# Kernel tuning notes

Measured on AMD Instinct MI355X. Metric: run time of the kernel, lower is better.

Reference implementation:

```python
import jax, jax.numpy as jnp
import numpy as np


def _binarize(x):
    # tf.where(x < 0, -1.0, 1.0)
    return jnp.where(x < 0, -1.0, 1.0).astype(jnp.float32)


def setup_inputs() -> dict:
    key = jax.random.key(0)
    k1, k2, k3 = jax.random.split(key, 3)
    M, K, N = 8192, 2048, 2048
    inputs = jax.random.normal(k1, (M, K), dtype=jnp.float32)
    kernel = jax.random.normal(k2, (K, N), dtype=jnp.float32) * 0.1
    bias = jax.random.normal(k3, (N,), dtype=jnp.float32) * 0.01
    return {"inputs": inputs, "kernel": kernel, "bias": bias}


def reference(inputs, kernel, bias):
    bx = _binarize(inputs)          # [M, K] in {-1, +1}
    bw = _binarize(kernel)          # [K, N] in {-1, +1}
    return jnp.matmul(bx, bw) + bias  # [M, N]
```

## Files before the change

### kernel.cpp

```cpp
#include <hip/hip_runtime.h>
#include <stdint.h>

typedef __attribute__((ext_vector_type(4))) int int4v;
typedef __attribute__((ext_vector_type(8))) int int8v;
typedef __attribute__((ext_vector_type(4))) float floatx4;
typedef __attribute__((ext_vector_type(16))) unsigned char uchar16;

#define MDIM 8192
#define KDIM 2048
#define NDIM 2048
#define BM 256
#define BN 256
#define KB 1024
#define BKB 128
#define NT 8

__device__ __forceinline__ void load16_lds(const void* g, void* l) {
  __builtin_amdgcn_global_load_lds(
      (const __attribute__((address_space(1))) void*)g,
      (__attribute__((address_space(3))) void*)l, 16, 0, 0);
}

#define XBLK 2048
#define WBLK 512

__global__ void binarize_fused(const float* __restrict__ X,
                               const float* __restrict__ W,
                               unsigned char* __restrict__ Xb,
                               unsigned char* __restrict__ WbT) {
  const int b = blockIdx.x;
  if (b < XBLK) {
    size_t i = ((size_t)b * 256 + threadIdx.x) * 32;
    const float4* xp = (const float4*)(X + i);
    uchar16 o;
#pragma unroll
    for (int h = 0; h < 8; ++h) {
      float4 a = xp[h];
      unsigned n0 = (a.x < 0.f) ? 0xAu : 0x2u;
      unsigned n1 = (a.y < 0.f) ? 0xAu : 0x2u;
      unsigned n2 = (a.z < 0.f) ? 0xAu : 0x2u;
      unsigned n3 = (a.w < 0.f) ? 0xAu : 0x2u;
      o[2 * h]     = (unsigned char)(n0 | (n1 << 4));
      o[2 * h + 1] = (unsigned char)(n2 | (n3 << 4));
    }
    *(uchar16*)(Xb + i / 2) = o;
  } else {
    const int bw = b - XBLK;
    const int nb = bw & 31;
    const int kb = bw >> 5;
    const int nn = threadIdx.x & 63;
    const int kc = kb * 4 + (threadIdx.x >> 6);
    const float* wp = W + (size_t)(kc * 32) * NDIM + nb * 64 + nn;
    uchar16 o;
#pragma unroll
    for (int j = 0; j < 16; ++j) {
      unsigned lo = (wp[(size_t)(2 * j) * NDIM] < 0.f) ? 0xAu : 0x2u;
      unsigned hi = (wp[(size_t)(2 * j + 1) * NDIM] < 0.f) ? 0xAu : 0x2u;
      o[j] = (unsigned char)(lo | (hi << 4));
    }
    *(uchar16*)(WbT + (size_t)(nb * 64 + nn) * KB + kc * 16) = o;
  }
}

__global__ __launch_bounds__(512, 2) void gemm_bin_fp4(
    const unsigned char* __restrict__ A,
    const unsigned char* __restrict__ B,
    const float* __restrict__ bias,
    float* __restrict__ C) {
  __shared__ __align__(16) unsigned char As[2][BM * BKB];
  __shared__ __align__(16) unsigned char Bs[2][BN * BKB];

  const int tid = threadIdx.x;
  const int lane = tid & 63;
  const int wv = tid >> 6;
  const int wm = wv >> 2;
  const int wn = wv & 3;
  const int r = lane & 15;
  const int q = lane >> 4;

  const int m0 = blockIdx.x * BM;
  const int n0 = blockIdx.y * BN;

  floatx4 acc[8][4] = {};

  const int qbase = wv * 256;
  int srcoff[4];
#pragma unroll
  for (int i = 0; i < 4; ++i) {
    const int s = qbase + i * 64 + lane;
    const int row = s >> 3;
    const int cg = (s & 7) ^ (row & 7);
    srcoff[i] = row * KB + cg * 16;
  }
  const unsigned char* Ab = A + (size_t)m0 * KB;
  const unsigned char* Bb = B + (size_t)n0 * KB;

#pragma unroll
  for (int i = 0; i < 4; ++i) {
    load16_lds(Ab + srcoff[i], &As[0][(qbase + i * 64) * 16]);
    load16_lds(Bb + srcoff[i], &Bs[0][(qbase + i * 64) * 16]);
  }

  for (int t = 0; t < NT; ++t) {
    const int cur = t & 1;
    if (t < NT - 1) {
      const int kbb = (t + 1) * BKB;
#pragma unroll
      for (int i = 0; i < 4; ++i) {
        load16_lds(Ab + kbb + srcoff[i], &As[cur ^ 1][(qbase + i * 64) * 16]);
        load16_lds(Bb + kbb + srcoff[i], &Bs[cur ^ 1][(qbase + i * 64) * 16]);
      }
      asm volatile("s_waitcnt vmcnt(8)" ::: "memory");
    } else {
      asm volatile("s_waitcnt vmcnt(0)" ::: "memory");
    }
    __builtin_amdgcn_s_barrier();

#pragma unroll
    for (int s2 = 0; s2 < 2; ++s2) {
      int8v b8[4];
#pragma unroll
      for (int tn = 0; tn < 4; ++tn) {
        const int brow = wn * 64 + tn * 16 + r;
        int4v bv = *(const int4v*)(&Bs[cur][brow * BKB + (((s2 * 4 + q) ^ (r & 7)) * 16)]);
        b8[tn] = int8v{bv[0], bv[1], bv[2], bv[3], 0, 0, 0, 0};
      }
#pragma unroll
      for (int tm = 0; tm < 8; ++tm) {
        const int arow = wm * 128 + tm * 16 + r;
        int4v av = *(const int4v*)(&As[cur][arow * BKB + (((s2 * 4 + q) ^ (r & 7)) * 16)]);
        int8v a8 = int8v{av[0], av[1], av[2], av[3], 0, 0, 0, 0};
#pragma unroll
        for (int tn = 0; tn < 4; ++tn)
          acc[tm][tn] = __builtin_amdgcn_mfma_scale_f32_16x16x128_f8f6f4(
              a8, b8[tn], acc[tm][tn], 4, 4,
              0, 0x7F7F7F7F, 0, 0x7F7F7F7F);
      }
    }
    asm volatile("s_waitcnt lgkmcnt(0)" ::: "memory");
    __builtin_amdgcn_s_barrier();
  }

  __syncthreads();
  float* slab = (float*)(&As[0][0]) + wv * 1024;

  float bv[4];
#pragma unroll
  for (int tn = 0; tn < 4; ++tn) bv[tn] = bias[n0 + wn * 64 + tn * 16 + r];

  const int lrow = lane >> 4;
  const int lc4 = lane & 15;

#pragma unroll
  for (int tm = 0; tm < 8; ++tm) {
#pragma unroll
    for (int tn = 0; tn < 4; ++tn)
#pragma unroll
      for (int v = 0; v < 4; ++v)
        slab[(q * 4 + v) * 64 + tn * 16 + r] = acc[tm][tn][v] + bv[tn];
    asm volatile("s_waitcnt lgkmcnt(0)" ::: "memory");
    __builtin_amdgcn_sched_barrier(0);
#pragma unroll
    for (int j = 0; j < 4; ++j) {
      const int row = j * 4 + lrow;
      floatx4 val = *(const floatx4*)(&slab[row * 64 + lc4 * 4]);
      *(floatx4*)(&C[(size_t)(m0 + wm * 128 + tm * 16 + row) * NDIM +
                     n0 + wn * 64 + lc4 * 4]) = val;
    }
    asm volatile("s_waitcnt lgkmcnt(0)" ::: "memory");
    __builtin_amdgcn_sched_barrier(0);
  }
}

extern "C" void kernel_launch(void* const* d_in, const int* in_sizes, int n_in,
                              void* d_out, int out_size, void* d_ws, size_t ws_size,
                              hipStream_t stream) {
  const float* X = (const float*)d_in[0];
  const float* W = (const float*)d_in[1];
  const float* bias = (const float*)d_in[2];
  float* out = (float*)d_out;

  unsigned char* Xb = (unsigned char*)d_ws;
  unsigned char* WbT = Xb + (size_t)MDIM * KDIM / 2;

  binarize_fused<<<dim3(XBLK + WBLK), 256, 0, stream>>>(X, W, Xb, WbT);
  gemm_bin_fp4<<<dim3(MDIM / BM, NDIM / BN), 512, 0, stream>>>(Xb, WbT, bias, out);
}
```

Baseline: 143.8 us.

## Interleave next-tile global loads with MFMA phases and pad epilogue LDS slab

Splits each K-tile iteration into four phases, each with fragment loads, part of the next tile's global-to-LDS prefetch, and a 4x4 MFMA block. The phases are separated by barriers and raised wave priority during the MFMA bursts, so memory traffic is spread across compute instead of issued all at once. Waiting moves to vmcnt(0) at the start of each tile. The epilogue LDS slab row stride is padded from 64 to 68 floats to reduce bank conflicts. The extra barriers per tile may add synchronisation cost.

```diff
diff --git a/kernel.cpp b/kernel.cpp
--- a/kernel.cpp
+++ b/kernel.cpp
@@ -103,46 +103,112 @@
 
   for (int t = 0; t < NT; ++t) {
     const int cur = t & 1;
-    if (t < NT - 1) {
-      const int kbb = (t + 1) * BKB;
-#pragma unroll
-      for (int i = 0; i < 4; ++i) {
-        load16_lds(Ab + kbb + srcoff[i], &As[cur ^ 1][(qbase + i * 64) * 16]);
-        load16_lds(Bb + kbb + srcoff[i], &Bs[cur ^ 1][(qbase + i * 64) * 16]);
-      }
-      asm volatile("s_waitcnt vmcnt(8)" ::: "memory");
-    } else {
-      asm volatile("s_waitcnt vmcnt(0)" ::: "memory");
-    }
-    __builtin_amdgcn_s_barrier();
-
-#pragma unroll
-    for (int s2 = 0; s2 < 2; ++s2) {
-      int8v b8[4];
-#pragma unroll
-      for (int tn = 0; tn < 4; ++tn) {
-        const int brow = wn * 64 + tn * 16 + r;
-        int4v bv = *(const int4v*)(&Bs[cur][brow * BKB + (((s2 * 4 + q) ^ (r & 7)) * 16)]);
-        b8[tn] = int8v{bv[0], bv[1], bv[2], bv[3], 0, 0, 0, 0};
-      }
-#pragma unroll
-      for (int tm = 0; tm < 8; ++tm) {
-        const int arow = wm * 128 + tm * 16 + r;
-        int4v av = *(const int4v*)(&As[cur][arow * BKB + (((s2 * 4 + q) ^ (r & 7)) * 16)]);
-        int8v a8 = int8v{av[0], av[1], av[2], av[3], 0, 0, 0, 0};
-#pragma unroll
-        for (int tn = 0; tn < 4; ++tn)
-          acc[tm][tn] = __builtin_amdgcn_mfma_scale_f32_16x16x128_f8f6f4(
-              a8, b8[tn], acc[tm][tn], 4, 4,
-              0, 0x7F7F7F7F, 0, 0x7F7F7F7F);
-      }
-    }
-    asm volatile("s_waitcnt lgkmcnt(0)" ::: "memory");
-    __builtin_amdgcn_s_barrier();
+    const int kbb = (t + 1) * BKB;
+    const bool pf = (t < NT - 1);
+
+    asm volatile("s_waitcnt vmcnt(0)" ::: "memory");
+    __builtin_amdgcn_s_barrier();
+
+    int8v b8[4], a8[4];
+    const int cs0 = (q ^ (r & 7)) * 16;
+    const int cs1 = ((4 + q) ^ (r & 7)) * 16;
+
+#pragma unroll
+    for (int tn = 0; tn < 4; ++tn) {
+      int4v v = *(const int4v*)(&Bs[cur][(wn * 64 + tn * 16 + r) * BKB + cs0]);
+      b8[tn] = int8v{v[0], v[1], v[2], v[3], 0, 0, 0, 0};
+    }
+#pragma unroll
+    for (int tm = 0; tm < 4; ++tm) {
+      int4v v = *(const int4v*)(&As[cur][(wm * 128 + tm * 16 + r) * BKB + cs0]);
+      a8[tm] = int8v{v[0], v[1], v[2], v[3], 0, 0, 0, 0};
+    }
+    if (pf) {
+      load16_lds(Ab + kbb + srcoff[0], &As[cur ^ 1][(qbase + 0 * 64) * 16]);
+      load16_lds(Ab + kbb + srcoff[1], &As[cur ^ 1][(qbase + 1 * 64) * 16]);
+    }
+    asm volatile("s_waitcnt lgkmcnt(0)" ::: "memory");
+    __builtin_amdgcn_sched_barrier(0);
+    __builtin_amdgcn_s_setprio(1);
+#pragma unroll
+    for (int tm = 0; tm < 4; ++tm)
+#pragma unroll
+      for (int tn = 0; tn < 4; ++tn)
+        acc[tm][tn] = __builtin_amdgcn_mfma_scale_f32_16x16x128_f8f6f4(
+            a8[tm], b8[tn], acc[tm][tn], 4, 4, 0, 0x7F7F7F7F, 0, 0x7F7F7F7F);
+    __builtin_amdgcn_s_setprio(0);
+    __builtin_amdgcn_s_barrier();
+
+#pragma unroll
+    for (int tm = 0; tm < 4; ++tm) {
+      int4v v = *(const int4v*)(&As[cur][(wm * 128 + (tm + 4) * 16 + r) * BKB + cs0]);
+      a8[tm] = int8v{v[0], v[1], v[2], v[3], 0, 0, 0, 0};
+    }
+    if (pf) {
+      load16_lds(Ab + kbb + srcoff[2], &As[cur ^ 1][(qbase + 2 * 64) * 16]);
+      load16_lds(Ab + kbb + srcoff[3], &As[cur ^ 1][(qbase + 3 * 64) * 16]);
+    }
+    asm volatile("s_waitcnt lgkmcnt(0)" ::: "memory");
+    __builtin_amdgcn_sched_barrier(0);
+    __builtin_amdgcn_s_setprio(1);
+#pragma unroll
+    for (int tm = 0; tm < 4; ++tm)
+#pragma unroll
+      for (int tn = 0; tn < 4; ++tn)
+        acc[tm + 4][tn] = __builtin_amdgcn_mfma_scale_f32_16x16x128_f8f6f4(
+            a8[tm], b8[tn], acc[tm + 4][tn], 4, 4, 0, 0x7F7F7F7F, 0, 0x7F7F7F7F);
+    __builtin_amdgcn_s_setprio(0);
+    __builtin_amdgcn_s_barrier();
+
+#pragma unroll
+    for (int tn = 0; tn < 4; ++tn) {
+      int4v v = *(const int4v*)(&Bs[cur][(wn * 64 + tn * 16 + r) * BKB + cs1]);
+      b8[tn] = int8v{v[0], v[1], v[2], v[3], 0, 0, 0, 0};
+    }
+#pragma unroll
+    for (int tm = 0; tm < 4; ++tm) {
+      int4v v = *(const int4v*)(&As[cur][(wm * 128 + tm * 16 + r) * BKB + cs1]);
+      a8[tm] = int8v{v[0], v[1], v[2], v[3], 0, 0, 0, 0};
+    }
+    if (pf) {
+      load16_lds(Bb + kbb + srcoff[0], &Bs[cur ^ 1][(qbase + 0 * 64) * 16]);
+      load16_lds(Bb + kbb + srcoff[1], &Bs[cur ^ 1][(qbase + 1 * 64) * 16]);
+    }
+    asm volatile("s_waitcnt lgkmcnt(0)" ::: "memory");
+    __builtin_amdgcn_sched_barrier(0);
+    __builtin_amdgcn_s_setprio(1);
+#pragma unroll
+    for (int tm = 0; tm < 4; ++tm)
+#pragma unroll
+      for (int tn = 0; tn < 4; ++tn)
+        acc[tm][tn] = __builtin_amdgcn_mfma_scale_f32_16x16x128_f8f6f4(
+            a8[tm], b8[tn], acc[tm][tn], 4, 4, 0, 0x7F7F7F7F, 0, 0x7F7F7F7F);
+    __builtin_amdgcn_s_setprio(0);
+    __builtin_amdgcn_s_barrier();
+
+#pragma unroll
+    for (int tm = 0; tm < 4; ++tm) {
+      int4v v = *(const int4v*)(&As[cur][(wm * 128 + (tm + 4) * 16 + r) * BKB + cs1]);
+      a8[tm] = int8v{v[0], v[1], v[2], v[3], 0, 0, 0, 0};
+    }
+    if (pf) {
+      load16_lds(Bb + kbb + srcoff[2], &Bs[cur ^ 1][(qbase + 2 * 64) * 16]);
+      load16_lds(Bb + kbb + srcoff[3], &Bs[cur ^ 1][(qbase + 3 * 64) * 16]);
+    }
+    asm volatile("s_waitcnt lgkmcnt(0)" ::: "memory");
+    __builtin_amdgcn_sched_barrier(0);
+    __builtin_amdgcn_s_setprio(1);
+#pragma unroll
+    for (int tm = 0; tm < 4; ++tm)
+#pragma unroll
+      for (int tn = 0; tn < 4; ++tn)
+        acc[tm + 4][tn] = __builtin_amdgcn_mfma_scale_f32_16x16x128_f8f6f4(
+            a8[tm], b8[tn], acc[tm + 4][tn], 4, 4, 0, 0x7F7F7F7F, 0, 0x7F7F7F7F);
+    __builtin_amdgcn_s_setprio(0);
   }
 
   __syncthreads();
-  float* slab = (float*)(&As[0][0]) + wv * 1024;
+  float* slab = (float*)(&As[0][0]) + wv * 1088;
 
   float bv[4];
 #pragma unroll
@@ -157,13 +223,13 @@
     for (int tn = 0; tn < 4; ++tn)
 #pragma unroll
       for (int v = 0; v < 4; ++v)
-        slab[(q * 4 + v) * 64 + tn * 16 + r] = acc[tm][tn][v] + bv[tn];
+        slab[(q * 4 + v) * 68 + tn * 16 + r] = acc[tm][tn][v] + bv[tn];
     asm volatile("s_waitcnt lgkmcnt(0)" ::: "memory");
     __builtin_amdgcn_sched_barrier(0);
 #pragma unroll
     for (int j = 0; j < 4; ++j) {
       const int row = j * 4 + lrow;
-      floatx4 val = *(const floatx4*)(&slab[row * 64 + lc4 * 4]);
+      floatx4 val = *(const floatx4*)(&slab[row * 68 + lc4 * 4]);
       *(floatx4*)(&C[(size_t)(m0 + wm * 128 + tm * 16 + row) * NDIM +
                      n0 + wn * 64 + lc4 * 4]) = val;
     }
```

Result: no change. 143.3 us (-0.4%).

## Switch to 32x32x64 FP4 MFMA with interleaved prefetch and padded epilogue

Applied to the files above, without the earlier changes.

Replaces the 16x16x128 scaled MFMA tiling with 32x32x64 tiles (4x2 per wave, 16-float accumulators). Each K block is split into four sub-steps, and the next block's global-to-LDS loads are spread across them. Barriers sit between sub-steps and setprio is raised around the MFMA bursts. The epilogue stages results through a padded LDS slab (stride 68) split across both A and B buffers. The intent is fewer LDS fragment reads per FLOP and better overlap of loads with MFMA, at the cost of more barriers and a full vmcnt(0) wait at the top of each iteration.

```diff
diff --git a/kernel.cpp b/kernel.cpp
--- a/kernel.cpp
+++ b/kernel.cpp
@@ -4,6 +4,7 @@
 typedef __attribute__((ext_vector_type(4))) int int4v;
 typedef __attribute__((ext_vector_type(8))) int int8v;
 typedef __attribute__((ext_vector_type(4))) float floatx4;
+typedef __attribute__((ext_vector_type(16))) float floatx16;
 typedef __attribute__((ext_vector_type(16))) unsigned char uchar16;
 
 #define MDIM 8192
@@ -75,13 +76,13 @@
   const int wv = tid >> 6;
   const int wm = wv >> 2;
   const int wn = wv & 3;
-  const int r = lane & 15;
-  const int q = lane >> 4;
+  const int rl = lane & 31;
+  const int h = lane >> 5;
 
   const int m0 = blockIdx.x * BM;
   const int n0 = blockIdx.y * BN;
 
-  floatx4 acc[8][4] = {};
+  floatx16 acc[4][2] = {};
 
   const int qbase = wv * 256;
   int srcoff[4];
@@ -103,69 +104,82 @@
 
   for (int t = 0; t < NT; ++t) {
     const int cur = t & 1;
-    if (t < NT - 1) {
-      const int kbb = (t + 1) * BKB;
-#pragma unroll
-      for (int i = 0; i < 4; ++i) {
-        load16_lds(Ab + kbb + srcoff[i], &As[cur ^ 1][(qbase + i * 64) * 16]);
-        load16_lds(Bb + kbb + srcoff[i], &Bs[cur ^ 1][(qbase + i * 64) * 16]);
-      }
-      asm volatile("s_waitcnt vmcnt(8)" ::: "memory");
-    } else {
-      asm volatile("s_waitcnt vmcnt(0)" ::: "memory");
-    }
+    const int kbb = (t + 1) * BKB;
+    const bool pf = (t < NT - 1);
+
+    asm volatile("s_waitcnt vmcnt(0)" ::: "memory");
     __builtin_amdgcn_s_barrier();
 
 #pragma unroll
-    for (int s2 = 0; s2 < 2; ++s2) {
-      int8v b8[4];
-#pragma unroll
-      for (int tn = 0; tn < 4; ++tn) {
-        const int brow = wn * 64 + tn * 16 + r;
-        int4v bv = *(const int4v*)(&Bs[cur][brow * BKB + (((s2 * 4 + q) ^ (r & 7)) * 16)]);
-        b8[tn] = int8v{bv[0], bv[1], bv[2], bv[3], 0, 0, 0, 0};
-      }
-#pragma unroll
-      for (int tm = 0; tm < 8; ++tm) {
-        const int arow = wm * 128 + tm * 16 + r;
-        int4v av = *(const int4v*)(&As[cur][arow * BKB + (((s2 * 4 + q) ^ (r & 7)) * 16)]);
-        int8v a8 = int8v{av[0], av[1], av[2], av[3], 0, 0, 0, 0};
-#pragma unroll
-        for (int tn = 0; tn < 4; ++tn)
-          acc[tm][tn] = __builtin_amdgcn_mfma_scale_f32_16x16x128_f8f6f4(
-              a8, b8[tn], acc[tm][tn], 4, 4,
-              0, 0x7F7F7F7F, 0, 0x7F7F7F7F);
-      }
-    }
-    asm volatile("s_waitcnt lgkmcnt(0)" ::: "memory");
-    __builtin_amdgcn_s_barrier();
+    for (int s3 = 0; s3 < 4; ++s3) {
+      const int cswz = ((s3 * 2 + h) ^ (rl & 7)) * 16;
+      int8v a8[4], b8[2];
+#pragma unroll
+      for (int tn = 0; tn < 2; ++tn) {
+        int4v v = *(const int4v*)(&Bs[cur][(wn * 64 + tn * 32 + rl) * BKB + cswz]);
+        b8[tn] = int8v{v[0], v[1], v[2], v[3], 0, 0, 0, 0};
+      }
+#pragma unroll
+      for (int tm = 0; tm < 4; ++tm) {
+        int4v v = *(const int4v*)(&As[cur][(wm * 128 + tm * 32 + rl) * BKB + cswz]);
+        a8[tm] = int8v{v[0], v[1], v[2], v[3], 0, 0, 0, 0};
+      }
+      if (pf) {
+        if (s3 == 0) {
+          load16_lds(Ab + kbb + srcoff[0], &As[cur ^ 1][(qbase + 0 * 64) * 16]);
+          load16_lds(Ab + kbb + srcoff[1], &As[cur ^ 1][(qbase + 1 * 64) * 16]);
+        } else if (s3 == 1) {
+          load16_lds(Ab + kbb + srcoff[2], &As[cur ^ 1][(qbase + 2 * 64) * 16]);
+          load16_lds(Ab + kbb + srcoff[3], &As[cur ^ 1][(qbase + 3 * 64) * 16]);
+        } else if (s3 == 2) {
+          load16_lds(Bb + kbb + srcoff[0], &Bs[cur ^ 1][(qbase + 0 * 64) * 16]);
+          load16_lds(Bb + kbb + srcoff[1], &Bs[cur ^ 1][(qbase + 1 * 64) * 16]);
+        } else {
+          load16_lds(Bb + kbb + srcoff[2], &Bs[cur ^ 1][(qbase + 2 * 64) * 16]);
+          load16_lds(Bb + kbb + srcoff[3], &Bs[cur ^ 1][(qbase + 3 * 64) * 16]);
+        }
+      }
+      asm volatile("s_waitcnt lgkmcnt(0)" ::: "memory");
+      __builtin_amdgcn_sched_barrier(0);
+      __builtin_amdgcn_s_setprio(1);
+#pragma unroll
+      for (int tm = 0; tm < 4; ++tm)
+#pragma unroll
+        for (int tn = 0; tn < 2; ++tn)
+          acc[tm][tn] = __builtin_amdgcn_mfma_scale_f32_32x32x64_f8f6f4(
+              a8[tm], b8[tn], acc[tm][tn], 4, 4, 0, 0x7F7F7F7F, 0, 0x7F7F7F7F);
+      __builtin_amdgcn_s_setprio(0);
+      if (s3 < 3) __builtin_amdgcn_s_barrier();
+    }
   }
 
   __syncthreads();
-  float* slab = (float*)(&As[0][0]) + wv * 1024;
-
-  float bv[4];
-#pragma unroll
-  for (int tn = 0; tn < 4; ++tn) bv[tn] = bias[n0 + wn * 64 + tn * 16 + r];
-
-  const int lrow = lane >> 4;
-  const int lc4 = lane & 15;
-
-#pragma unroll
-  for (int tm = 0; tm < 8; ++tm) {
-#pragma unroll
-    for (int tn = 0; tn < 4; ++tn)
-#pragma unroll
-      for (int v = 0; v < 4; ++v)
-        slab[(q * 4 + v) * 64 + tn * 16 + r] = acc[tm][tn][v] + bv[tn];
+  float* slab = ((wv < 4) ? (float*)&As[0][0] : (float*)&Bs[0][0]) + (wv & 3) * (32 * 68);
+
+  float bv[2];
+#pragma unroll
+  for (int tn = 0; tn < 2; ++tn) bv[tn] = bias[n0 + wn * 64 + tn * 32 + rl];
+
+  const int jrow = lane >> 4;
+  const int c4 = lane & 15;
+
+#pragma unroll
+  for (int tm = 0; tm < 4; ++tm) {
+#pragma unroll
+    for (int tn = 0; tn < 2; ++tn)
+#pragma unroll
+      for (int reg = 0; reg < 16; ++reg) {
+        const int rowi = (reg & 3) + 8 * (reg >> 2) + 4 * h;
+        slab[rowi * 68 + tn * 32 + rl] = acc[tm][tn][reg] + bv[tn];
+      }
     asm volatile("s_waitcnt lgkmcnt(0)" ::: "memory");
     __builtin_amdgcn_sched_barrier(0);
 #pragma unroll
-    for (int j = 0; j < 4; ++j) {
-      const int row = j * 4 + lrow;
-      floatx4 val = *(const floatx4*)(&slab[row * 64 + lc4 * 4]);
-      *(floatx4*)(&C[(size_t)(m0 + wm * 128 + tm * 16 + row) * NDIM +
-                     n0 + wn * 64 + lc4 * 4]) = val;
+    for (int j = 0; j < 8; ++j) {
+      const int row = j * 4 + jrow;
+      floatx4 val = *(const floatx4*)(&slab[row * 68 + c4 * 4]);
+      *(floatx4*)(&C[(size_t)(m0 + wm * 128 + tm * 32 + row) * NDIM +
+                     n0 + wn * 64 + c4 * 4]) = val;
     }
     asm volatile("s_waitcnt lgkmcnt(0)" ::: "memory");
     __builtin_amdgcn_sched_barrier(0);
```

Measured after the change: 145.5 us. Within noise of the previous version (+1.2%).
